# Performance work log

Hardware: AMD Instinct MI355X
Metric: run time of the kernel (lower is better)

## Reference

```python
import jax, jax.numpy as jnp
import numpy as np

B, T, D = 2, 2048, 1024
H, HS = 16, 64
EPS = 1e-5

def _ln(x, g, b):
    m = jnp.mean(x, axis=-1, keepdims=True)
    v = jnp.mean((x - m) ** 2, axis=-1, keepdims=True)
    return (x - m) * jax.lax.rsqrt(v + EPS) * g + b

def setup_inputs() -> dict:
    key = jax.random.key(0)
    ks = jax.random.split(key, 8)
    s_in = 1.0 / np.sqrt(D)
    s_ff = 1.0 / np.sqrt(4 * D)
    return {
        "embds": jax.random.normal(ks[0], (B, T, D), jnp.float32),
        "Wq": jax.random.normal(ks[1], (H, D, HS), jnp.float32) * s_in,
        "Wk": jax.random.normal(ks[2], (H, D, HS), jnp.float32) * s_in,
        "Wv": jax.random.normal(ks[3], (H, D, HS), jnp.float32) * s_in,
        "ln1_g": jnp.ones((D,), jnp.float32),
        "ln1_b": jnp.zeros((D,), jnp.float32),
        "ln2_g": jnp.ones((D,), jnp.float32),
        "ln2_b": jnp.zeros((D,), jnp.float32),
        "W1": jax.random.normal(ks[4], (D, 4 * D), jnp.float32) * s_in,
        "b1": jnp.zeros((4 * D,), jnp.float32),
        "W2": jax.random.normal(ks[5], (4 * D, D), jnp.float32) * s_ff,
        "b2": jnp.zeros((D,), jnp.float32),
    }

def reference(embds, Wq, Wk, Wv, ln1_g, ln1_b, ln2_g, ln2_b, W1, b1, W2, b2):
    _, t, d = embds.shape
    x = _ln(embds, ln1_g, ln1_b)
    q = jnp.einsum("btd,hde->bhte", x, Wq)
    k = jnp.einsum("btd,hde->bhte", x, Wk)
    v = jnp.einsum("btd,hde->bhte", x, Wv)
    # NOTE: repo scales by num_embds**-0.5 (C of input), not head_size**-0.5
    scores = jnp.einsum("bhte,bhse->bhts", q, k) * (d ** -0.5)
    causal = jnp.tril(jnp.ones((t, t), bool))
    scores = jnp.where(causal, scores, -jnp.inf)
    w = jax.nn.softmax(scores, axis=-1)
    o = jnp.einsum("bhts,bhse->bhte", w, v)  # [B,H,T,HS]
    attn = o.transpose(0, 2, 1, 3).reshape(embds.shape[0], t, -1)  # concat heads
    embds = embds + attn
    y = _ln(embds, ln2_g, ln2_b)
    ff = jax.nn.relu(y @ W1 + b1) @ W2 + b2
    return embds + ff
```

## Files before the change

### kernel.cpp

```cpp
#include <hip/hip_runtime.h>

using s16x8 = __attribute__((ext_vector_type(8))) short;
using f32x4 = __attribute__((ext_vector_type(4))) float;
typedef unsigned int   u32;
typedef unsigned short u16;

__device__ __forceinline__ u16 f2bf(float f) {
  u32 u = __float_as_uint(f);
  u += 0x7fffu + ((u >> 16) & 1u);
  return (u16)(u >> 16);
}
__device__ __forceinline__ float bf2f(u16 s) {
  return __uint_as_float(((u32)s) << 16);
}

typedef __attribute__((address_space(1))) const unsigned int g_u32;
typedef __attribute__((address_space(3))) unsigned int l_u32;
__device__ __forceinline__ void gload16(const void* g, void* l) {
  __builtin_amdgcn_global_load_lds((g_u32*)g, (l_u32*)l, 16, 0, 0);
}

#define WAITB(N) asm volatile("s_waitcnt vmcnt(" #N ")\ns_barrier" ::: "memory")
#define BAR()    asm volatile("s_barrier" ::: "memory")

__device__ __forceinline__ size_t kfrag_addr(int bh, int t, int e) {
  const int pair = (((t >> 4) & 3) << 1) + (e >> 5);
  const int slot = ((e >> 3) & 3) * 16 + (t & 15);
  return ((((size_t)bh * 32 + (t >> 6)) * 8 + pair) * 64 + slot) * 8 + (e & 7);
}
__device__ __forceinline__ size_t vfrag_addr(int bh, int t, int e) {
  const int pair = (((e >> 4) & 3) << 1) + ((t >> 5) & 1);
  const int slot = ((t >> 3) & 3) * 16 + (e & 15);
  return ((((size_t)bh * 32 + (t >> 6)) * 8 + pair) * 64 + slot) * 8 + (t & 7);
}

__global__ __launch_bounds__(256) void transpose_pack(
    const float* __restrict__ src, u16* __restrict__ dst, int R, int C)
{
  __shared__ u16 tile[64][66];
  const int tid = threadIdx.x;
  const int c0 = blockIdx.x * 64, r0 = blockIdx.y * 64;
  const size_t zoff = (size_t)blockIdx.z * R * C;
  src += zoff; dst += zoff;
  const int rr = tid >> 6, cc = tid & 63;
  #pragma unroll
  for (int i = 0; i < 16; ++i)
    tile[i * 4 + rr][cc] = f2bf(src[(size_t)(r0 + i * 4 + rr) * C + c0 + cc]);
  __syncthreads();
  #pragma unroll
  for (int i = 0; i < 16; ++i)
    dst[(size_t)(c0 + i * 4 + rr) * R + r0 + cc] = tile[cc][i * 4 + rr];
}

__global__ __launch_bounds__(256) void transpose_qkv(
    const float* __restrict__ Wq, const float* __restrict__ Wk,
    const float* __restrict__ Wv, u16* __restrict__ dst)
{
  __shared__ u16 tile[64][66];
  const int tid = threadIdx.x;
  const int sel = blockIdx.z >> 4, head = blockIdx.z & 15;
  const int r0 = blockIdx.y * 64;
  const float* src = ((sel == 0) ? Wq : (sel == 1) ? Wk : Wv) + (size_t)head * 65536;
  u16* d = dst + ((size_t)sel << 20) + (size_t)head * 65536;
  const int rr = tid >> 6, cc = tid & 63;
  #pragma unroll
  for (int i = 0; i < 16; ++i)
    tile[i * 4 + rr][cc] = f2bf(src[(size_t)(r0 + i * 4 + rr) * 64 + cc]);
  __syncthreads();
  #pragma unroll
  for (int i = 0; i < 16; ++i)
    d[(size_t)(i * 4 + rr) * 1024 + r0 + cc] = tile[cc][i * 4 + rr];
}

__global__ __launch_bounds__(256) void ln_kernel(
    const float* __restrict__ x, const float* __restrict__ g,
    const float* __restrict__ be, u16* __restrict__ out)
{
  const int row = blockIdx.x, tid = threadIdx.x;
  const int lane = tid & 63, wave = tid >> 6;
  const float4 v = ((const float4*)(x + (size_t)row * 1024))[tid];
  float s  = v.x + v.y + v.z + v.w;
  float sq = v.x * v.x + v.y * v.y + v.z * v.z + v.w * v.w;
  #pragma unroll
  for (int m = 1; m < 64; m <<= 1) { s += __shfl_xor(s, m); sq += __shfl_xor(sq, m); }
  __shared__ float rs[4], rq[4];
  if (lane == 0) { rs[wave] = s; rq[wave] = sq; }
  __syncthreads();
  s  = rs[0] + rs[1] + rs[2] + rs[3];
  sq = rq[0] + rq[1] + rq[2] + rq[3];
  const float mean = s * (1.0f / 1024.0f);
  const float var  = sq * (1.0f / 1024.0f) - mean * mean;
  const float rstd = rsqrtf(var + 1e-5f);
  const int c = tid * 4;
  const float4 gv = ((const float4*)g)[tid];
  const float4 bv = ((const float4*)be)[tid];
  ushort4 o;
  o.x = f2bf((v.x - mean) * rstd * gv.x + bv.x);
  o.y = f2bf((v.y - mean) * rstd * gv.y + bv.y);
  o.z = f2bf((v.z - mean) * rstd * gv.z + bv.z);
  o.w = f2bf((v.w - mean) * rstd * gv.w + bv.w);
  *(ushort4*)&out[(size_t)row * 1024 + c] = o;
}

#define MFMA_Q(MQ, NH)                                                        \
  do {                                                                        \
    __builtin_amdgcn_s_setprio(1);                                            \
    _Pragma("unroll") for (int m_ = 0; m_ < 4; ++m_)                          \
      _Pragma("unroll") for (int n_ = 0; n_ < 2; ++n_)                        \
        _Pragma("unroll") for (int ks_ = 0; ks_ < 2; ++ks_)                   \
          acc[MQ * 4 + m_][NH * 2 + n_] =                                     \
            __builtin_amdgcn_mfma_f32_16x16x32_bf16(                          \
              aF[m_][ks_], (NH ? b1F : b0F)[n_][ks_],                         \
              acc[MQ * 4 + m_][NH * 2 + n_], 0, 0, 0);                        \
    __builtin_amdgcn_s_setprio(0);                                            \
  } while (0)

template<int MODE>
__global__ __launch_bounds__(512, 2) void gemm256(
    const u16* __restrict__ A, int lda, const u16* __restrict__ BT, int ldb,
    int K, u16* __restrict__ o1, const float* __restrict__ bias,
    u16* __restrict__ pout)
{
  __shared__ alignas(16) u16 lds[2][2][256 * 64];
  const int tid = threadIdx.x, lane = tid & 63, w = tid >> 6;
  const int wm = w >> 2, wn = w & 3;
  const int fr = lane & 15, g = lane >> 4;
  const int gx = gridDim.x, nwg = gx * gridDim.y;
  int lid = blockIdx.y * gx + blockIdx.x;
  lid = (lid & 7) * (nwg >> 3) + (lid >> 3);
  const int col0 = (lid % gx) * 256, row0 = (lid / gx) * 256;
  const int koff = (MODE == 3) ? blockIdx.z * 1024 : 0;
  if constexpr (MODE == 3) pout += (size_t)blockIdx.z * (4096 * 1024);

  const int srow = w * 16 + (lane >> 3);
  const int scol8 = (lane & 7) ^ ((lane >> 3) & 7);
  const u16* Ab = A  + (size_t)(row0 + srow) * lda + koff + scol8 * 8;
  const u16* Bb = BT + (size_t)(col0 + srow) * ldb + koff + scol8 * 8;
  const int sdst = (w * 16) * 64 + lane * 8;

  const int x7 = fr & 7;
  const int rA = wm * 128 + fr;
  const int rB = wn * 64 + fr;

  f32x4 acc[8][4] = {};
  s16x8 aF[4][2], b0F[2][2], b1F[2][2];
  const int nkt = K >> 6;

  auto stA = [&](int buf, int half, int kt) {
    #pragma unroll
    for (int g2 = 0; g2 < 2; ++g2)
      gload16(Ab + (size_t)(half * 128 + g2 * 8) * lda + kt * 64,
              &lds[buf][0][(half * 128 + g2 * 8) * 64 + sdst]);
  };
  auto stB = [&](int buf, int half, int kt) {
    #pragma unroll
    for (int g2 = 0; g2 < 2; ++g2)
      gload16(Bb + (size_t)(half * 128 + g2 * 8) * ldb + kt * 64,
              &lds[buf][1][(half * 128 + g2 * 8) * 64 + sdst]);
  };
  auto rdA = [&](int buf, int mq) {
    #pragma unroll
    for (int m = 0; m < 4; ++m)
      #pragma unroll
      for (int ks = 0; ks < 2; ++ks)
        aF[m][ks] = *(const s16x8*)
          &lds[buf][0][(rA + mq * 64 + m * 16) * 64 + ((ks * 4 + g) ^ x7) * 8];
  };
  auto rdB0 = [&](int buf) {
    #pragma unroll
    for (int n = 0; n < 2; ++n)
      #pragma unroll
      for (int ks = 0; ks < 2; ++ks)
        b0F[n][ks] = *(const s16x8*)
          &lds[buf][1][(rB + n * 16) * 64 + ((ks * 4 + g) ^ x7) * 8];
  };
  auto rdB1 = [&](int buf) {
    #pragma unroll
    for (int n = 0; n < 2; ++n)
      #pragma unroll
      for (int ks = 0; ks < 2; ++ks)
        b1F[n][ks] = *(const s16x8*)
          &lds[buf][1][(rB + (n + 2) * 16) * 64 + ((ks * 4 + g) ^ x7) * 8];
  };

  stA(0, 0, 0); stA(0, 1, 0); stB(0, 0, 0); stB(0, 1, 0);
  stA(1, 0, 1); stA(1, 1, 1); stB(1, 0, 1); stB(1, 1, 1);
  WAITB(8);

  const int niter = nkt >> 1;
  for (int i = 0; i < niter; ++i) {
    #pragma unroll
    for (int half = 0; half < 2; ++half) {
      const int buf = half;
      const int skt = 2 * i + 2 + half;
      const bool st = (skt < nkt);
      rdA(buf, 0); rdB0(buf);
      BAR();
      MFMA_Q(0, 0);
      BAR();
      rdB1(buf);
      if (st) stB(buf, 0, skt);
      BAR();
      MFMA_Q(0, 1);
      BAR();
      rdA(buf, 1);
      if (st) stA(buf, 0, skt);
      BAR();
      MFMA_Q(1, 0);
      BAR();
      if (st) { stA(buf, 1, skt); stB(buf, 1, skt); }
      BAR();
      MFMA_Q(1, 1);
      WAITB(6);
    }
  }

  #pragma unroll
  for (int m8 = 0; m8 < 8; ++m8) {
    const int rbase = row0 + wm * 128 + m8 * 16 + g * 4;
    #pragma unroll
    for (int n4 = 0; n4 < 4; ++n4) {
      const int col = col0 + wn * 64 + n4 * 16 + fr;
      if constexpr (MODE == 1) {
        const float bb = bias[col];
        #pragma unroll
        for (int j = 0; j < 4; ++j)
          o1[(size_t)(rbase + j) * 4096 + col] =
            f2bf(fmaxf(acc[m8][n4][j] + bb, 0.0f));
      } else {
        #pragma unroll
        for (int j = 0; j < 4; ++j)
          pout[(size_t)(rbase + j) * 1024 + col] = f2bf(acc[m8][n4][j]);
      }
    }
  }
}

__global__ __launch_bounds__(256) void ff2_reduce(
    const u16* __restrict__ pbuf, const float* __restrict__ e2,
    const float* __restrict__ b2, float* __restrict__ out)
{
  const int i4 = blockIdx.x * 256 + threadIdx.x;
  const int row = i4 >> 8, c4 = i4 & 255;
  float4 a = ((const float4*)e2)[i4];
  const float4 bb = ((const float4*)b2)[c4];
  a.x += bb.x; a.y += bb.y; a.z += bb.z; a.w += bb.w;
  #pragma unroll
  for (int z = 0; z < 4; ++z) {
    const ushort4 p = *(const ushort4*)
      &pbuf[(size_t)z * (4096 * 1024) + (size_t)row * 1024 + c4 * 4];
    a.x += bf2f(p.x); a.y += bf2f(p.y); a.z += bf2f(p.z); a.w += bf2f(p.w);
  }
  ((float4*)out)[i4] = a;
}

template<int MODE, int MR>
__global__ __launch_bounds__(256) void gemm128(
    const u16* __restrict__ A, const u16* __restrict__ BT, int K,
    u16* __restrict__ o0q, u16* __restrict__ o0k, u16* __restrict__ o0v,
    u16* __restrict__ o1, const float* __restrict__ bias,
    float* __restrict__ o2, const float* __restrict__ resid)
{
  constexpr int BM = 64 * MR;
  __shared__ alignas(16) u16 As[3][BM * 32];
  __shared__ alignas(16) u16 Bs[3][128 * 32];
  const int tid = threadIdx.x, lane = tid & 63, wave = tid >> 6;
  const int wr = wave >> 1, wc = wave & 1;
  const int gx = gridDim.x;
  const int nwg = gx * gridDim.y;
  int lid = blockIdx.y * gx + blockIdx.x;
  lid = (lid & 7) * (nwg >> 3) + (lid >> 3);
  const int row0 = (lid / gx) * BM, col0 = (lid % gx) * 128;
  const int fr = lane & 15, g = lane >> 4;
  const int swz = (g ^ ((fr >> 1) & 3)) * 8;

  const int sr = wave * 16 + (lane >> 2);
  const int sc = ((lane & 3) ^ ((lane >> 3) & 3)) * 8;
  const u16* Ap0 = A  + (size_t)(row0 + sr) * K + sc;
  const u16* Ap1 = A  + (size_t)(row0 + 64 + sr) * K + sc;
  const u16* Bp0 = BT + (size_t)(col0 + sr) * K + sc;
  const u16* Bp1 = BT + (size_t)(col0 + 64 + sr) * K + sc;

  f32x4 acc[2 * MR][4] = {};

  auto stage = [&](int sel, int k0) {
    gload16(Ap0 + k0, &As[sel][wave * 512]);
    if constexpr (MR == 2) gload16(Ap1 + k0, &As[sel][(4 + wave) * 512]);
    gload16(Bp0 + k0, &Bs[sel][wave * 512]);
    gload16(Bp1 + k0, &Bs[sel][(4 + wave) * 512]);
  };
  auto compute = [&](int sel) {
    s16x8 af[2 * MR], bfr[4];
    #pragma unroll
    for (int m = 0; m < 2 * MR; ++m)
      af[m] = *(const s16x8*)&As[sel][(wr * (32 * MR) + m * 16 + fr) * 32 + swz];
    #pragma unroll
    for (int n = 0; n < 4; ++n)
      bfr[n] = *(const s16x8*)&Bs[sel][(wc * 64 + n * 16 + fr) * 32 + swz];
    #pragma unroll
    for (int m = 0; m < 2 * MR; ++m)
      #pragma unroll
      for (int n = 0; n < 4; ++n)
        acc[m][n] = __builtin_amdgcn_mfma_f32_16x16x32_bf16(af[m], bfr[n], acc[m][n], 0, 0, 0);
  };

  const int nsteps = K / 32;
  stage(0, 0);
  stage(1, 32);
  int cur = 0;
  for (int t = 0; t < nsteps - 1; ++t) {
    if constexpr (MR == 2) WAITB(4); else WAITB(3);
    const int nxt = (cur == 2) ? 0 : cur + 1;
    const int nn  = (nxt == 2) ? 0 : nxt + 1;
    if (t + 2 < nsteps) stage(nn, (t + 2) * 32);
    compute(cur);
    cur = nxt;
  }
  WAITB(0);
  compute(cur);

  const float QSCALE = 0.03125f * 1.4426950408889634f;
  #pragma unroll
  for (int m = 0; m < 2 * MR; ++m) {
    const int rbase = row0 + wr * (32 * MR) + m * 16 + g * 4;
    #pragma unroll
    for (int n = 0; n < 4; ++n) {
      const int col = col0 + wc * 64 + n * 16 + fr;
      if constexpr (MODE == 0) {
        const int ww = col >> 10, h = (col >> 6) & 15, e = col & 63;
        const int b = rbase >> 11, t0 = rbase & 2047;
        const int bh = b * 16 + h;
        if (ww == 0) {
          #pragma unroll
          for (int j = 0; j < 4; ++j)
            o0q[((size_t)bh * 2048 + (t0 + j)) * 64 + e] = f2bf(acc[m][n][j] * QSCALE);
        } else if (ww == 1) {
          #pragma unroll
          for (int j = 0; j < 4; ++j)
            o0k[kfrag_addr(bh, t0 + j, e)] = f2bf(acc[m][n][j]);
        } else {
          ushort4 pk;
          pk.x = f2bf(acc[m][n][0]); pk.y = f2bf(acc[m][n][1]);
          pk.z = f2bf(acc[m][n][2]); pk.w = f2bf(acc[m][n][3]);
          *(ushort4*)&o0v[vfrag_addr(bh, t0, e)] = pk;
        }
      } else if constexpr (MODE == 1) {
        const float bb = bias[col];
        #pragma unroll
        for (int j = 0; j < 4; ++j) {
          float v = fmaxf(acc[m][n][j] + bb, 0.0f);
          o1[(size_t)(rbase + j) * 4096 + col] = f2bf(v);
        }
      } else {
        const float bb = bias[col];
        #pragma unroll
        for (int j = 0; j < 4; ++j) {
          const size_t ix = (size_t)(rbase + j) * 1024 + col;
          o2[ix] = acc[m][n][j] + bb + resid[ix];
        }
      }
    }
  }
}

__global__ __launch_bounds__(256) void attn_mfma(
    const u16* __restrict__ q, const u16* __restrict__ kfragG,
    const u16* __restrict__ vfragG, const float* __restrict__ embds,
    float* __restrict__ e2)
{
  __shared__ alignas(16) u16 kbuf[3][4096];
  __shared__ alignas(16) u16 vbuf[3][4096];
  __shared__ alignas(16) u16 p_sm[4][16][72];
  const int tid = threadIdx.x, lane = tid & 63, wave = tid >> 6;
  const int bh = blockIdx.x & 31;
  const int qb = 31 - (blockIdx.x >> 5);
  const int q0 = qb * 64 + wave * 16;
  const int b = bh >> 4, h = bh & 15;
  const int fr = lane & 15, g = lane >> 4;

  const u16* qp = q + ((size_t)bh * 2048 + q0 + fr) * 64 + g * 8;
  const s16x8 qf0 = *(const s16x8*)(qp);
  const s16x8 qf1 = *(const s16x8*)(qp + 32);

  f32x4 o_acc[4] = {};
  float lacc[4] = {};

  const size_t fragbase = (size_t)bh * 131072;
  const int p0 = wave * 2, p1 = wave * 2 + 1;
  const int nch = qb + 1;

  auto stage_kv = [&](int sel, int c) {
    const size_t cb = fragbase + (size_t)c * 4096;
    gload16(kfragG + cb + p0 * 512 + lane * 8, &kbuf[sel][p0 * 512]);
    gload16(kfragG + cb + p1 * 512 + lane * 8, &kbuf[sel][p1 * 512]);
    gload16(vfragG + cb + p0 * 512 + lane * 8, &vbuf[sel][p0 * 512]);
    gload16(vfragG + cb + p1 * 512 + lane * 8, &vbuf[sel][p1 * 512]);
  };
  auto compute = [&](int sel, int s0) {
    f32x4 sacc[4] = {};
    #pragma unroll
    for (int n = 0; n < 4; ++n) {
      const s16x8 kf0 = *(const s16x8*)&kbuf[sel][(n * 2 + 0) * 512 + lane * 8];
      const s16x8 kf1 = *(const s16x8*)&kbuf[sel][(n * 2 + 1) * 512 + lane * 8];
      sacc[n] = __builtin_amdgcn_mfma_f32_16x16x32_bf16(qf0, kf0, sacc[n], 0, 0, 0);
      sacc[n] = __builtin_amdgcn_mfma_f32_16x16x32_bf16(qf1, kf1, sacc[n], 0, 0, 0);
    }
    if (s0 + 63 > q0) {
      #pragma unroll
      for (int n = 0; n < 4; ++n) {
        const int s = s0 + n * 16 + fr;
        #pragma unroll
        for (int j = 0; j < 4; ++j)
          if (s > q0 + g * 4 + j) sacc[n][j] = -1e30f;
      }
    }
    float p[4][4];
    #pragma unroll
    for (int n = 0; n < 4; ++n)
      #pragma unroll
      for (int j = 0; j < 4; ++j) {
        p[n][j] = __builtin_amdgcn_exp2f(sacc[n][j]);
        lacc[j] += p[n][j];
      }
    #pragma unroll
    for (int n = 0; n < 4; ++n)
      #pragma unroll
      for (int j = 0; j < 4; ++j)
        p_sm[wave][g * 4 + j][n * 16 + fr] = f2bf(p[n][j]);
    const s16x8 pf0 = *(const s16x8*)&p_sm[wave][fr][g * 8];
    const s16x8 pf1 = *(const s16x8*)&p_sm[wave][fr][32 + g * 8];
    #pragma unroll
    for (int n = 0; n < 4; ++n) {
      const s16x8 vf0 = *(const s16x8*)&vbuf[sel][(n * 2 + 0) * 512 + lane * 8];
      const s16x8 vf1 = *(const s16x8*)&vbuf[sel][(n * 2 + 1) * 512 + lane * 8];
      o_acc[n] = __builtin_amdgcn_mfma_f32_16x16x32_bf16(pf0, vf0, o_acc[n], 0, 0, 0);
      o_acc[n] = __builtin_amdgcn_mfma_f32_16x16x32_bf16(pf1, vf1, o_acc[n], 0, 0, 0);
    }
  };

  stage_kv(0, 0);
  if (nch > 1) stage_kv(1, 1);
  int cur = 0;
  for (int t = 0; t < nch - 1; ++t) {
    WAITB(4);
    const int nxt = (cur == 2) ? 0 : cur + 1;
    const int nn  = (nxt == 2) ? 0 : nxt + 1;
    if (t + 2 < nch) stage_kv(nn, t + 2);
    compute(cur, t * 64);
    cur = nxt;
  }
  WAITB(0);
  compute(cur, (nch - 1) * 64);

  #pragma unroll
  for (int j = 0; j < 4; ++j) {
    #pragma unroll
    for (int mm = 1; mm < 16; mm <<= 1) lacc[j] += __shfl_xor(lacc[j], mm);
  }
  #pragma unroll
  for (int n = 0; n < 4; ++n) {
    #pragma unroll
    for (int j = 0; j < 4; ++j) {
      const int t = q0 + g * 4 + j;
      const size_t oi = ((size_t)b * 2048 + t) * 1024 + (size_t)h * 64 + n * 16 + fr;
      e2[oi] = embds[oi] + o_acc[n][j] / lacc[j];
    }
  }
}

extern "C" void kernel_launch(void* const* d_in, const int* in_sizes, int n_in,
                              void* d_out, int out_size, void* d_ws, size_t ws_size,
                              hipStream_t stream) {
  const float* embds = (const float*)d_in[0];
  const float* Wq    = (const float*)d_in[1];
  const float* Wk    = (const float*)d_in[2];
  const float* Wv    = (const float*)d_in[3];
  const float* ln1g  = (const float*)d_in[4];
  const float* ln1b  = (const float*)d_in[5];
  const float* ln2g  = (const float*)d_in[6];
  const float* ln2b  = (const float*)d_in[7];
  const float* W1    = (const float*)d_in[8];
  const float* b1    = (const float*)d_in[9];
  const float* W2    = (const float*)d_in[10];
  const float* b2    = (const float*)d_in[11];
  float* out = (float*)d_out;

  char* ws = (char*)d_ws;
  u16*   xln   = (u16*)(ws);
  u16*   pbuf  = (u16*)(ws);
  u16*   wqkvT = (u16*)(ws + (8ull  << 20));
  u16*   qbuf  = (u16*)(ws + (14ull << 20));
  u16*   kfrag = (u16*)(ws + (22ull << 20));
  u16*   vfrag = (u16*)(ws + (30ull << 20));
  float* e2    = (float*)(ws + (38ull << 20));
  u16*   ybuf  = (u16*)(ws + (54ull << 20));
  u16*   w1T   = (u16*)(ws + (62ull << 20));
  u16*   w2T   = (u16*)(ws + (70ull << 20));
  u16*   hid   = (u16*)(ws + (78ull << 20));

  transpose_qkv<<<dim3(1, 16, 48), 256, 0, stream>>>(Wq, Wk, Wv, wqkvT);
  transpose_pack<<<dim3(64, 16, 1), 256, 0, stream>>>(W1, w1T, 1024, 4096);
  transpose_pack<<<dim3(16, 64, 1), 256, 0, stream>>>(W2, w2T, 4096, 1024);
  ln_kernel<<<4096, 256, 0, stream>>>(embds, ln1g, ln1b, xln);
  gemm128<0, 2><<<dim3(24, 32), 256, 0, stream>>>(xln, wqkvT, 1024,
      qbuf, kfrag, vfrag, nullptr, nullptr, nullptr, nullptr);
  attn_mfma<<<1024, 256, 0, stream>>>(qbuf, kfrag, vfrag, embds, e2);
  ln_kernel<<<4096, 256, 0, stream>>>(e2, ln2g, ln2b, ybuf);
  gemm256<1><<<dim3(16, 16), 512, 0, stream>>>(ybuf, 1024, w1T, 1024, 1024,
      hid, b1, nullptr);
  gemm256<3><<<dim3(4, 16, 4), 512, 0, stream>>>(hid, 4096, w2T, 4096, 1024,
      nullptr, nullptr, pbuf);
  ff2_reduce<<<4096, 256, 0, stream>>>(pbuf, e2, b2, out);
}
```

Measured before the change: 190.6 us.

## Route QKV projection through gemm256 and widen attention blocks to 128 queries

The QKV projection now runs through the larger 256x256 gemm256 kernel with a new MODE 0 epilogue that scatters Q, K and V into their attention layouts, and the old gemm128 kernel is removed. The attention kernel now uses 512-thread blocks covering 128 query rows, so each staged K/V chunk is shared by 8 waves instead of 4. K/V buffering drops from triple to double, with a full wait at each step. The aim is more reuse of operands and fewer blocks, at the cost of a shallower prefetch pipeline in attention and a coarser grid (192 blocks) for the QKV GEMM.

```diff
diff --git a/kernel.cpp b/kernel.cpp
--- a/kernel.cpp
+++ b/kernel.cpp
@@ -119,7 +119,8 @@
 __global__ __launch_bounds__(512, 2) void gemm256(
     const u16* __restrict__ A, int lda, const u16* __restrict__ BT, int ldb,
     int K, u16* __restrict__ o1, const float* __restrict__ bias,
-    u16* __restrict__ pout)
+    u16* __restrict__ pout, u16* __restrict__ o0q, u16* __restrict__ o0k,
+    u16* __restrict__ o0v)
 {
   __shared__ alignas(16) u16 lds[2][2][256 * 64];
   const int tid = threadIdx.x, lane = tid & 63, w = tid >> 6;
@@ -215,13 +216,33 @@
     }
   }
 
+  const float QSCALE = 0.03125f * 1.4426950408889634f;
   #pragma unroll
   for (int m8 = 0; m8 < 8; ++m8) {
     const int rbase = row0 + wm * 128 + m8 * 16 + g * 4;
     #pragma unroll
     for (int n4 = 0; n4 < 4; ++n4) {
       const int col = col0 + wn * 64 + n4 * 16 + fr;
-      if constexpr (MODE == 1) {
+      if constexpr (MODE == 0) {
+        const int ww = col >> 10, h = (col >> 6) & 15, e = col & 63;
+        const int b = rbase >> 11, t0 = rbase & 2047;
+        const int bh = b * 16 + h;
+        if (ww == 0) {
+          #pragma unroll
+          for (int j = 0; j < 4; ++j)
+            o0q[((size_t)bh * 2048 + (t0 + j)) * 64 + e] =
+              f2bf(acc[m8][n4][j] * QSCALE);
+        } else if (ww == 1) {
+          #pragma unroll
+          for (int j = 0; j < 4; ++j)
+            o0k[kfrag_addr(bh, t0 + j, e)] = f2bf(acc[m8][n4][j]);
+        } else {
+          ushort4 pk;
+          pk.x = f2bf(acc[m8][n4][0]); pk.y = f2bf(acc[m8][n4][1]);
+          pk.z = f2bf(acc[m8][n4][2]); pk.w = f2bf(acc[m8][n4][3]);
+          *(ushort4*)&o0v[vfrag_addr(bh, t0, e)] = pk;
+        }
+      } else if constexpr (MODE == 1) {
         const float bb = bias[col];
         #pragma unroll
         for (int j = 0; j < 4; ++j)
@@ -254,127 +275,18 @@
   ((float4*)out)[i4] = a;
 }
 
-template<int MODE, int MR>
-__global__ __launch_bounds__(256) void gemm128(
-    const u16* __restrict__ A, const u16* __restrict__ BT, int K,
-    u16* __restrict__ o0q, u16* __restrict__ o0k, u16* __restrict__ o0v,
-    u16* __restrict__ o1, const float* __restrict__ bias,
-    float* __restrict__ o2, const float* __restrict__ resid)
-{
-  constexpr int BM = 64 * MR;
-  __shared__ alignas(16) u16 As[3][BM * 32];
-  __shared__ alignas(16) u16 Bs[3][128 * 32];
-  const int tid = threadIdx.x, lane = tid & 63, wave = tid >> 6;
-  const int wr = wave >> 1, wc = wave & 1;
-  const int gx = gridDim.x;
-  const int nwg = gx * gridDim.y;
-  int lid = blockIdx.y * gx + blockIdx.x;
-  lid = (lid & 7) * (nwg >> 3) + (lid >> 3);
-  const int row0 = (lid / gx) * BM, col0 = (lid % gx) * 128;
-  const int fr = lane & 15, g = lane >> 4;
-  const int swz = (g ^ ((fr >> 1) & 3)) * 8;
-
-  const int sr = wave * 16 + (lane >> 2);
-  const int sc = ((lane & 3) ^ ((lane >> 3) & 3)) * 8;
-  const u16* Ap0 = A  + (size_t)(row0 + sr) * K + sc;
-  const u16* Ap1 = A  + (size_t)(row0 + 64 + sr) * K + sc;
-  const u16* Bp0 = BT + (size_t)(col0 + sr) * K + sc;
-  const u16* Bp1 = BT + (size_t)(col0 + 64 + sr) * K + sc;
-
-  f32x4 acc[2 * MR][4] = {};
-
-  auto stage = [&](int sel, int k0) {
-    gload16(Ap0 + k0, &As[sel][wave * 512]);
-    if constexpr (MR == 2) gload16(Ap1 + k0, &As[sel][(4 + wave) * 512]);
-    gload16(Bp0 + k0, &Bs[sel][wave * 512]);
-    gload16(Bp1 + k0, &Bs[sel][(4 + wave) * 512]);
-  };
-  auto compute = [&](int sel) {
-    s16x8 af[2 * MR], bfr[4];
-    #pragma unroll
-    for (int m = 0; m < 2 * MR; ++m)
-      af[m] = *(const s16x8*)&As[sel][(wr * (32 * MR) + m * 16 + fr) * 32 + swz];
-    #pragma unroll
-    for (int n = 0; n < 4; ++n)
-      bfr[n] = *(const s16x8*)&Bs[sel][(wc * 64 + n * 16 + fr) * 32 + swz];
-    #pragma unroll
-    for (int m = 0; m < 2 * MR; ++m)
-      #pragma unroll
-      for (int n = 0; n < 4; ++n)
-        acc[m][n] = __builtin_amdgcn_mfma_f32_16x16x32_bf16(af[m], bfr[n], acc[m][n], 0, 0, 0);
-  };
-
-  const int nsteps = K / 32;
-  stage(0, 0);
-  stage(1, 32);
-  int cur = 0;
-  for (int t = 0; t < nsteps - 1; ++t) {
-    if constexpr (MR == 2) WAITB(4); else WAITB(3);
-    const int nxt = (cur == 2) ? 0 : cur + 1;
-    const int nn  = (nxt == 2) ? 0 : nxt + 1;
-    if (t + 2 < nsteps) stage(nn, (t + 2) * 32);
-    compute(cur);
-    cur = nxt;
-  }
-  WAITB(0);
-  compute(cur);
-
-  const float QSCALE = 0.03125f * 1.4426950408889634f;
-  #pragma unroll
-  for (int m = 0; m < 2 * MR; ++m) {
-    const int rbase = row0 + wr * (32 * MR) + m * 16 + g * 4;
-    #pragma unroll
-    for (int n = 0; n < 4; ++n) {
-      const int col = col0 + wc * 64 + n * 16 + fr;
-      if constexpr (MODE == 0) {
-        const int ww = col >> 10, h = (col >> 6) & 15, e = col & 63;
-        const int b = rbase >> 11, t0 = rbase & 2047;
-        const int bh = b * 16 + h;
-        if (ww == 0) {
-          #pragma unroll
-          for (int j = 0; j < 4; ++j)
-            o0q[((size_t)bh * 2048 + (t0 + j)) * 64 + e] = f2bf(acc[m][n][j] * QSCALE);
-        } else if (ww == 1) {
-          #pragma unroll
-          for (int j = 0; j < 4; ++j)
-            o0k[kfrag_addr(bh, t0 + j, e)] = f2bf(acc[m][n][j]);
-        } else {
-          ushort4 pk;
-          pk.x = f2bf(acc[m][n][0]); pk.y = f2bf(acc[m][n][1]);
-          pk.z = f2bf(acc[m][n][2]); pk.w = f2bf(acc[m][n][3]);
-          *(ushort4*)&o0v[vfrag_addr(bh, t0, e)] = pk;
-        }
-      } else if constexpr (MODE == 1) {
-        const float bb = bias[col];
-        #pragma unroll
-        for (int j = 0; j < 4; ++j) {
-          float v = fmaxf(acc[m][n][j] + bb, 0.0f);
-          o1[(size_t)(rbase + j) * 4096 + col] = f2bf(v);
-        }
-      } else {
-        const float bb = bias[col];
-        #pragma unroll
-        for (int j = 0; j < 4; ++j) {
-          const size_t ix = (size_t)(rbase + j) * 1024 + col;
-          o2[ix] = acc[m][n][j] + bb + resid[ix];
-        }
-      }
-    }
-  }
-}
-
-__global__ __launch_bounds__(256) void attn_mfma(
+__global__ __launch_bounds__(512, 6) void attn_mfma(
     const u16* __restrict__ q, const u16* __restrict__ kfragG,
     const u16* __restrict__ vfragG, const float* __restrict__ embds,
     float* __restrict__ e2)
 {
-  __shared__ alignas(16) u16 kbuf[3][4096];
-  __shared__ alignas(16) u16 vbuf[3][4096];
-  __shared__ alignas(16) u16 p_sm[4][16][72];
+  __shared__ alignas(16) u16 kbuf[2][4096];
+  __shared__ alignas(16) u16 vbuf[2][4096];
+  __shared__ alignas(16) u16 p_sm[8][16][72];
   const int tid = threadIdx.x, lane = tid & 63, wave = tid >> 6;
   const int bh = blockIdx.x & 31;
-  const int qb = 31 - (blockIdx.x >> 5);
-  const int q0 = qb * 64 + wave * 16;
+  const int qb = 15 - (blockIdx.x >> 5);
+  const int q0 = qb * 128 + wave * 16;
   const int b = bh >> 4, h = bh & 15;
   const int fr = lane & 15, g = lane >> 4;
 
@@ -386,15 +298,12 @@
   float lacc[4] = {};
 
   const size_t fragbase = (size_t)bh * 131072;
-  const int p0 = wave * 2, p1 = wave * 2 + 1;
-  const int nch = qb + 1;
+  const int nch = qb * 2 + 2;
 
   auto stage_kv = [&](int sel, int c) {
     const size_t cb = fragbase + (size_t)c * 4096;
-    gload16(kfragG + cb + p0 * 512 + lane * 8, &kbuf[sel][p0 * 512]);
-    gload16(kfragG + cb + p1 * 512 + lane * 8, &kbuf[sel][p1 * 512]);
-    gload16(vfragG + cb + p0 * 512 + lane * 8, &vbuf[sel][p0 * 512]);
-    gload16(vfragG + cb + p1 * 512 + lane * 8, &vbuf[sel][p1 * 512]);
+    gload16(kfragG + cb + wave * 512 + lane * 8, &kbuf[sel][wave * 512]);
+    gload16(vfragG + cb + wave * 512 + lane * 8, &vbuf[sel][wave * 512]);
   };
   auto compute = [&](int sel, int s0) {
     f32x4 sacc[4] = {};
@@ -414,19 +323,14 @@
           if (s > q0 + g * 4 + j) sacc[n][j] = -1e30f;
       }
     }
-    float p[4][4];
     #pragma unroll
     for (int n = 0; n < 4; ++n)
       #pragma unroll
       for (int j = 0; j < 4; ++j) {
-        p[n][j] = __builtin_amdgcn_exp2f(sacc[n][j]);
-        lacc[j] += p[n][j];
+        const float pe = __builtin_amdgcn_exp2f(sacc[n][j]);
+        lacc[j] += pe;
+        p_sm[wave][g * 4 + j][n * 16 + fr] = f2bf(pe);
       }
-    #pragma unroll
-    for (int n = 0; n < 4; ++n)
-      #pragma unroll
-      for (int j = 0; j < 4; ++j)
-        p_sm[wave][g * 4 + j][n * 16 + fr] = f2bf(p[n][j]);
     const s16x8 pf0 = *(const s16x8*)&p_sm[wave][fr][g * 8];
     const s16x8 pf1 = *(const s16x8*)&p_sm[wave][fr][32 + g * 8];
     #pragma unroll
@@ -439,18 +343,11 @@
   };
 
   stage_kv(0, 0);
-  if (nch > 1) stage_kv(1, 1);
-  int cur = 0;
-  for (int t = 0; t < nch - 1; ++t) {
-    WAITB(4);
-    const int nxt = (cur == 2) ? 0 : cur + 1;
-    const int nn  = (nxt == 2) ? 0 : nxt + 1;
-    if (t + 2 < nch) stage_kv(nn, t + 2);
-    compute(cur, t * 64);
-    cur = nxt;
-  }
-  WAITB(0);
-  compute(cur, (nch - 1) * 64);
+  for (int t = 0; t < nch; ++t) {
+    WAITB(0);
+    if (t + 1 < nch) stage_kv((t + 1) & 1, t + 1);
+    compute(t & 1, t * 64);
+  }
 
   #pragma unroll
   for (int j = 0; j < 4; ++j) {
@@ -502,13 +399,13 @@
   transpose_pack<<<dim3(64, 16, 1), 256, 0, stream>>>(W1, w1T, 1024, 4096);
   transpose_pack<<<dim3(16, 64, 1), 256, 0, stream>>>(W2, w2T, 4096, 1024);
   ln_kernel<<<4096, 256, 0, stream>>>(embds, ln1g, ln1b, xln);
-  gemm128<0, 2><<<dim3(24, 32), 256, 0, stream>>>(xln, wqkvT, 1024,
-      qbuf, kfrag, vfrag, nullptr, nullptr, nullptr, nullptr);
-  attn_mfma<<<1024, 256, 0, stream>>>(qbuf, kfrag, vfrag, embds, e2);
+  gemm256<0><<<dim3(12, 16), 512, 0, stream>>>(xln, 1024, wqkvT, 1024, 1024,
+      nullptr, nullptr, nullptr, qbuf, kfrag, vfrag);
+  attn_mfma<<<512, 512, 0, stream>>>(qbuf, kfrag, vfrag, embds, e2);
   ln_kernel<<<4096, 256, 0, stream>>>(e2, ln2g, ln2b, ybuf);
   gemm256<1><<<dim3(16, 16), 512, 0, stream>>>(ybuf, 1024, w1T, 1024, 1024,
-      hid, b1, nullptr);
+      hid, b1, nullptr, nullptr, nullptr, nullptr);
   gemm256<3><<<dim3(4, 16, 4), 512, 0, stream>>>(hid, 4096, w2T, 4096, 1024,
-      nullptr, nullptr, pbuf);
+      nullptr, nullptr, pbuf, nullptr, nullptr, nullptr);
   ff2_reduce<<<4096, 256, 0, stream>>>(pbuf, e2, b2, out);
 }
```

Measured after the change: 191.5 us. No clear change (+0.4%).

## Double attention query tile to 128 rows with 8 waves and double-buffered KV

Applied to the files above, without the earlier changes.

The attention kernel now runs 512 threads (8 waves) per block, covering 128 query rows instead of 64, so each staged K/V chunk is shared by twice as many waves. The KV pipeline drops from triple to double buffering with a full wait each iteration, and each wave issues one load per K and V chunk. The exp/store loop is fused so probabilities go straight to LDS. This halves global K/V traffic per query but weakens prefetch depth, and for the diagonal block the extra chunk is computed fully masked for half the waves. The gemm256 and reduce kernels were only moved in the file.

```diff
diff --git a/kernel.cpp b/kernel.cpp
--- a/kernel.cpp
+++ b/kernel.cpp
@@ -100,158 +100,6 @@
   o.z = f2bf((v.z - mean) * rstd * gv.z + bv.z);
   o.w = f2bf((v.w - mean) * rstd * gv.w + bv.w);
   *(ushort4*)&out[(size_t)row * 1024 + c] = o;
-}
-
-#define MFMA_Q(MQ, NH)                                                        \
-  do {                                                                        \
-    __builtin_amdgcn_s_setprio(1);                                            \
-    _Pragma("unroll") for (int m_ = 0; m_ < 4; ++m_)                          \
-      _Pragma("unroll") for (int n_ = 0; n_ < 2; ++n_)                        \
-        _Pragma("unroll") for (int ks_ = 0; ks_ < 2; ++ks_)                   \
-          acc[MQ * 4 + m_][NH * 2 + n_] =                                     \
-            __builtin_amdgcn_mfma_f32_16x16x32_bf16(                          \
-              aF[m_][ks_], (NH ? b1F : b0F)[n_][ks_],                         \
-              acc[MQ * 4 + m_][NH * 2 + n_], 0, 0, 0);                        \
-    __builtin_amdgcn_s_setprio(0);                                            \
-  } while (0)
-
-template<int MODE>
-__global__ __launch_bounds__(512, 2) void gemm256(
-    const u16* __restrict__ A, int lda, const u16* __restrict__ BT, int ldb,
-    int K, u16* __restrict__ o1, const float* __restrict__ bias,
-    u16* __restrict__ pout)
-{
-  __shared__ alignas(16) u16 lds[2][2][256 * 64];
-  const int tid = threadIdx.x, lane = tid & 63, w = tid >> 6;
-  const int wm = w >> 2, wn = w & 3;
-  const int fr = lane & 15, g = lane >> 4;
-  const int gx = gridDim.x, nwg = gx * gridDim.y;
-  int lid = blockIdx.y * gx + blockIdx.x;
-  lid = (lid & 7) * (nwg >> 3) + (lid >> 3);
-  const int col0 = (lid % gx) * 256, row0 = (lid / gx) * 256;
-  const int koff = (MODE == 3) ? blockIdx.z * 1024 : 0;
-  if constexpr (MODE == 3) pout += (size_t)blockIdx.z * (4096 * 1024);
-
-  const int srow = w * 16 + (lane >> 3);
-  const int scol8 = (lane & 7) ^ ((lane >> 3) & 7);
-  const u16* Ab = A  + (size_t)(row0 + srow) * lda + koff + scol8 * 8;
-  const u16* Bb = BT + (size_t)(col0 + srow) * ldb + koff + scol8 * 8;
-  const int sdst = (w * 16) * 64 + lane * 8;
-
-  const int x7 = fr & 7;
-  const int rA = wm * 128 + fr;
-  const int rB = wn * 64 + fr;
-
-  f32x4 acc[8][4] = {};
-  s16x8 aF[4][2], b0F[2][2], b1F[2][2];
-  const int nkt = K >> 6;
-
-  auto stA = [&](int buf, int half, int kt) {
-    #pragma unroll
-    for (int g2 = 0; g2 < 2; ++g2)
-      gload16(Ab + (size_t)(half * 128 + g2 * 8) * lda + kt * 64,
-              &lds[buf][0][(half * 128 + g2 * 8) * 64 + sdst]);
-  };
-  auto stB = [&](int buf, int half, int kt) {
-    #pragma unroll
-    for (int g2 = 0; g2 < 2; ++g2)
-      gload16(Bb + (size_t)(half * 128 + g2 * 8) * ldb + kt * 64,
-              &lds[buf][1][(half * 128 + g2 * 8) * 64 + sdst]);
-  };
-  auto rdA = [&](int buf, int mq) {
-    #pragma unroll
-    for (int m = 0; m < 4; ++m)
-      #pragma unroll
-      for (int ks = 0; ks < 2; ++ks)
-        aF[m][ks] = *(const s16x8*)
-          &lds[buf][0][(rA + mq * 64 + m * 16) * 64 + ((ks * 4 + g) ^ x7) * 8];
-  };
-  auto rdB0 = [&](int buf) {
-    #pragma unroll
-    for (int n = 0; n < 2; ++n)
-      #pragma unroll
-      for (int ks = 0; ks < 2; ++ks)
-        b0F[n][ks] = *(const s16x8*)
-          &lds[buf][1][(rB + n * 16) * 64 + ((ks * 4 + g) ^ x7) * 8];
-  };
-  auto rdB1 = [&](int buf) {
-    #pragma unroll
-    for (int n = 0; n < 2; ++n)
-      #pragma unroll
-      for (int ks = 0; ks < 2; ++ks)
-        b1F[n][ks] = *(const s16x8*)
-          &lds[buf][1][(rB + (n + 2) * 16) * 64 + ((ks * 4 + g) ^ x7) * 8];
-  };
-
-  stA(0, 0, 0); stA(0, 1, 0); stB(0, 0, 0); stB(0, 1, 0);
-  stA(1, 0, 1); stA(1, 1, 1); stB(1, 0, 1); stB(1, 1, 1);
-  WAITB(8);
-
-  const int niter = nkt >> 1;
-  for (int i = 0; i < niter; ++i) {
-    #pragma unroll
-    for (int half = 0; half < 2; ++half) {
-      const int buf = half;
-      const int skt = 2 * i + 2 + half;
-      const bool st = (skt < nkt);
-      rdA(buf, 0); rdB0(buf);
-      BAR();
-      MFMA_Q(0, 0);
-      BAR();
-      rdB1(buf);
-      if (st) stB(buf, 0, skt);
-      BAR();
-      MFMA_Q(0, 1);
-      BAR();
-      rdA(buf, 1);
-      if (st) stA(buf, 0, skt);
-      BAR();
-      MFMA_Q(1, 0);
-      BAR();
-      if (st) { stA(buf, 1, skt); stB(buf, 1, skt); }
-      BAR();
-      MFMA_Q(1, 1);
-      WAITB(6);
-    }
-  }
-
-  #pragma unroll
-  for (int m8 = 0; m8 < 8; ++m8) {
-    const int rbase = row0 + wm * 128 + m8 * 16 + g * 4;
-    #pragma unroll
-    for (int n4 = 0; n4 < 4; ++n4) {
-      const int col = col0 + wn * 64 + n4 * 16 + fr;
-      if constexpr (MODE == 1) {
-        const float bb = bias[col];
-        #pragma unroll
-        for (int j = 0; j < 4; ++j)
-          o1[(size_t)(rbase + j) * 4096 + col] =
-            f2bf(fmaxf(acc[m8][n4][j] + bb, 0.0f));
-      } else {
-        #pragma unroll
-        for (int j = 0; j < 4; ++j)
-          pout[(size_t)(rbase + j) * 1024 + col] = f2bf(acc[m8][n4][j]);
-      }
-    }
-  }
-}
-
-__global__ __launch_bounds__(256) void ff2_reduce(
-    const u16* __restrict__ pbuf, const float* __restrict__ e2,
-    const float* __restrict__ b2, float* __restrict__ out)
-{
-  const int i4 = blockIdx.x * 256 + threadIdx.x;
-  const int row = i4 >> 8, c4 = i4 & 255;
-  float4 a = ((const float4*)e2)[i4];
-  const float4 bb = ((const float4*)b2)[c4];
-  a.x += bb.x; a.y += bb.y; a.z += bb.z; a.w += bb.w;
-  #pragma unroll
-  for (int z = 0; z < 4; ++z) {
-    const ushort4 p = *(const ushort4*)
-      &pbuf[(size_t)z * (4096 * 1024) + (size_t)row * 1024 + c4 * 4];
-    a.x += bf2f(p.x); a.y += bf2f(p.y); a.z += bf2f(p.z); a.w += bf2f(p.w);
-  }
-  ((float4*)out)[i4] = a;
 }
 
 template<int MODE, int MR>
@@ -363,18 +211,170 @@
   }
 }
 
-__global__ __launch_bounds__(256) void attn_mfma(
+#define MFMA_Q(MQ, NH)                                                        \
+  do {                                                                        \
+    __builtin_amdgcn_s_setprio(1);                                            \
+    _Pragma("unroll") for (int m_ = 0; m_ < 4; ++m_)                          \
+      _Pragma("unroll") for (int n_ = 0; n_ < 2; ++n_)                        \
+        _Pragma("unroll") for (int ks_ = 0; ks_ < 2; ++ks_)                   \
+          acc[MQ * 4 + m_][NH * 2 + n_] =                                     \
+            __builtin_amdgcn_mfma_f32_16x16x32_bf16(                          \
+              aF[m_][ks_], (NH ? b1F : b0F)[n_][ks_],                         \
+              acc[MQ * 4 + m_][NH * 2 + n_], 0, 0, 0);                        \
+    __builtin_amdgcn_s_setprio(0);                                            \
+  } while (0)
+
+template<int MODE>
+__global__ __launch_bounds__(512, 2) void gemm256(
+    const u16* __restrict__ A, int lda, const u16* __restrict__ BT, int ldb,
+    int K, u16* __restrict__ o1, const float* __restrict__ bias,
+    u16* __restrict__ pout)
+{
+  __shared__ alignas(16) u16 lds[2][2][256 * 64];
+  const int tid = threadIdx.x, lane = tid & 63, w = tid >> 6;
+  const int wm = w >> 2, wn = w & 3;
+  const int fr = lane & 15, g = lane >> 4;
+  const int gx = gridDim.x, nwg = gx * gridDim.y;
+  int lid = blockIdx.y * gx + blockIdx.x;
+  lid = (lid & 7) * (nwg >> 3) + (lid >> 3);
+  const int col0 = (lid % gx) * 256, row0 = (lid / gx) * 256;
+  const int koff = (MODE == 3) ? blockIdx.z * 1024 : 0;
+  if constexpr (MODE == 3) pout += (size_t)blockIdx.z * (4096 * 1024);
+
+  const int srow = w * 16 + (lane >> 3);
+  const int scol8 = (lane & 7) ^ ((lane >> 3) & 7);
+  const u16* Ab = A  + (size_t)(row0 + srow) * lda + koff + scol8 * 8;
+  const u16* Bb = BT + (size_t)(col0 + srow) * ldb + koff + scol8 * 8;
+  const int sdst = (w * 16) * 64 + lane * 8;
+
+  const int x7 = fr & 7;
+  const int rA = wm * 128 + fr;
+  const int rB = wn * 64 + fr;
+
+  f32x4 acc[8][4] = {};
+  s16x8 aF[4][2], b0F[2][2], b1F[2][2];
+  const int nkt = K >> 6;
+
+  auto stA = [&](int buf, int half, int kt) {
+    #pragma unroll
+    for (int g2 = 0; g2 < 2; ++g2)
+      gload16(Ab + (size_t)(half * 128 + g2 * 8) * lda + kt * 64,
+              &lds[buf][0][(half * 128 + g2 * 8) * 64 + sdst]);
+  };
+  auto stB = [&](int buf, int half, int kt) {
+    #pragma unroll
+    for (int g2 = 0; g2 < 2; ++g2)
+      gload16(Bb + (size_t)(half * 128 + g2 * 8) * ldb + kt * 64,
+              &lds[buf][1][(half * 128 + g2 * 8) * 64 + sdst]);
+  };
+  auto rdA = [&](int buf, int mq) {
+    #pragma unroll
+    for (int m = 0; m < 4; ++m)
+      #pragma unroll
+      for (int ks = 0; ks < 2; ++ks)
+        aF[m][ks] = *(const s16x8*)
+          &lds[buf][0][(rA + mq * 64 + m * 16) * 64 + ((ks * 4 + g) ^ x7) * 8];
+  };
+  auto rdB0 = [&](int buf) {
+    #pragma unroll
+    for (int n = 0; n < 2; ++n)
+      #pragma unroll
+      for (int ks = 0; ks < 2; ++ks)
+        b0F[n][ks] = *(const s16x8*)
+          &lds[buf][1][(rB + n * 16) * 64 + ((ks * 4 + g) ^ x7) * 8];
+  };
+  auto rdB1 = [&](int buf) {
+    #pragma unroll
+    for (int n = 0; n < 2; ++n)
+      #pragma unroll
+      for (int ks = 0; ks < 2; ++ks)
+        b1F[n][ks] = *(const s16x8*)
+          &lds[buf][1][(rB + (n + 2) * 16) * 64 + ((ks * 4 + g) ^ x7) * 8];
+  };
+
+  stA(0, 0, 0); stA(0, 1, 0); stB(0, 0, 0); stB(0, 1, 0);
+  stA(1, 0, 1); stA(1, 1, 1); stB(1, 0, 1); stB(1, 1, 1);
+  WAITB(8);
+
+  const int niter = nkt >> 1;
+  for (int i = 0; i < niter; ++i) {
+    #pragma unroll
+    for (int half = 0; half < 2; ++half) {
+      const int buf = half;
+      const int skt = 2 * i + 2 + half;
+      const bool st = (skt < nkt);
+      rdA(buf, 0); rdB0(buf);
+      BAR();
+      MFMA_Q(0, 0);
+      BAR();
+      rdB1(buf);
+      if (st) stB(buf, 0, skt);
+      BAR();
+      MFMA_Q(0, 1);
+      BAR();
+      rdA(buf, 1);
+      if (st) stA(buf, 0, skt);
+      BAR();
+      MFMA_Q(1, 0);
+      BAR();
+      if (st) { stA(buf, 1, skt); stB(buf, 1, skt); }
+      BAR();
+      MFMA_Q(1, 1);
+      WAITB(6);
+    }
+  }
+
+  #pragma unroll
+  for (int m8 = 0; m8 < 8; ++m8) {
+    const int rbase = row0 + wm * 128 + m8 * 16 + g * 4;
+    #pragma unroll
+    for (int n4 = 0; n4 < 4; ++n4) {
+      const int col = col0 + wn * 64 + n4 * 16 + fr;
+      if constexpr (MODE == 1) {
+        const float bb = bias[col];
+        #pragma unroll
+        for (int j = 0; j < 4; ++j)
+          o1[(size_t)(rbase + j) * 4096 + col] =
+            f2bf(fmaxf(acc[m8][n4][j] + bb, 0.0f));
+      } else {
+        #pragma unroll
+        for (int j = 0; j < 4; ++j)
+          pout[(size_t)(rbase + j) * 1024 + col] = f2bf(acc[m8][n4][j]);
+      }
+    }
+  }
+}
+
+__global__ __launch_bounds__(256) void ff2_reduce(
+    const u16* __restrict__ pbuf, const float* __restrict__ e2,
+    const float* __restrict__ b2, float* __restrict__ out)
+{
+  const int i4 = blockIdx.x * 256 + threadIdx.x;
+  const int row = i4 >> 8, c4 = i4 & 255;
+  float4 a = ((const float4*)e2)[i4];
+  const float4 bb = ((const float4*)b2)[c4];
+  a.x += bb.x; a.y += bb.y; a.z += bb.z; a.w += bb.w;
+  #pragma unroll
+  for (int z = 0; z < 4; ++z) {
+    const ushort4 p = *(const ushort4*)
+      &pbuf[(size_t)z * (4096 * 1024) + (size_t)row * 1024 + c4 * 4];
+    a.x += bf2f(p.x); a.y += bf2f(p.y); a.z += bf2f(p.z); a.w += bf2f(p.w);
+  }
+  ((float4*)out)[i4] = a;
+}
+
+__global__ __launch_bounds__(512, 6) void attn_mfma(
     const u16* __restrict__ q, const u16* __restrict__ kfragG,
     const u16* __restrict__ vfragG, const float* __restrict__ embds,
     float* __restrict__ e2)
 {
-  __shared__ alignas(16) u16 kbuf[3][4096];
-  __shared__ alignas(16) u16 vbuf[3][4096];
-  __shared__ alignas(16) u16 p_sm[4][16][72];
+  __shared__ alignas(16) u16 kbuf[2][4096];
+  __shared__ alignas(16) u16 vbuf[2][4096];
+  __shared__ alignas(16) u16 p_sm[8][16][72];
   const int tid = threadIdx.x, lane = tid & 63, wave = tid >> 6;
   const int bh = blockIdx.x & 31;
-  const int qb = 31 - (blockIdx.x >> 5);
-  const int q0 = qb * 64 + wave * 16;
+  const int qb = 15 - (blockIdx.x >> 5);
+  const int q0 = qb * 128 + wave * 16;
   const int b = bh >> 4, h = bh & 15;
   const int fr = lane & 15, g = lane >> 4;
 
@@ -386,15 +386,12 @@
   float lacc[4] = {};
 
   const size_t fragbase = (size_t)bh * 131072;
-  const int p0 = wave * 2, p1 = wave * 2 + 1;
-  const int nch = qb + 1;
+  const int nch = qb * 2 + 2;
 
   auto stage_kv = [&](int sel, int c) {
     const size_t cb = fragbase + (size_t)c * 4096;
-    gload16(kfragG + cb + p0 * 512 + lane * 8, &kbuf[sel][p0 * 512]);
-    gload16(kfragG + cb + p1 * 512 + lane * 8, &kbuf[sel][p1 * 512]);
-    gload16(vfragG + cb + p0 * 512 + lane * 8, &vbuf[sel][p0 * 512]);
-    gload16(vfragG + cb + p1 * 512 + lane * 8, &vbuf[sel][p1 * 512]);
+    gload16(kfragG + cb + wave * 512 + lane * 8, &kbuf[sel][wave * 512]);
+    gload16(vfragG + cb + wave * 512 + lane * 8, &vbuf[sel][wave * 512]);
   };
   auto compute = [&](int sel, int s0) {
     f32x4 sacc[4] = {};
@@ -414,19 +411,14 @@
           if (s > q0 + g * 4 + j) sacc[n][j] = -1e30f;
       }
     }
-    float p[4][4];
     #pragma unroll
     for (int n = 0; n < 4; ++n)
       #pragma unroll
       for (int j = 0; j < 4; ++j) {
-        p[n][j] = __builtin_amdgcn_exp2f(sacc[n][j]);
-        lacc[j] += p[n][j];
+        const float pe = __builtin_amdgcn_exp2f(sacc[n][j]);
+        lacc[j] += pe;
+        p_sm[wave][g * 4 + j][n * 16 + fr] = f2bf(pe);
       }
-    #pragma unroll
-    for (int n = 0; n < 4; ++n)
-      #pragma unroll
-      for (int j = 0; j < 4; ++j)
-        p_sm[wave][g * 4 + j][n * 16 + fr] = f2bf(p[n][j]);
     const s16x8 pf0 = *(const s16x8*)&p_sm[wave][fr][g * 8];
     const s16x8 pf1 = *(const s16x8*)&p_sm[wave][fr][32 + g * 8];
     #pragma unroll
@@ -439,18 +431,11 @@
   };
 
   stage_kv(0, 0);
-  if (nch > 1) stage_kv(1, 1);
-  int cur = 0;
-  for (int t = 0; t < nch - 1; ++t) {
-    WAITB(4);
-    const int nxt = (cur == 2) ? 0 : cur + 1;
-    const int nn  = (nxt == 2) ? 0 : nxt + 1;
-    if (t + 2 < nch) stage_kv(nn, t + 2);
-    compute(cur, t * 64);
-    cur = nxt;
-  }
-  WAITB(0);
-  compute(cur, (nch - 1) * 64);
+  for (int t = 0; t < nch; ++t) {
+    WAITB(0);
+    if (t + 1 < nch) stage_kv((t + 1) & 1, t + 1);
+    compute(t & 1, t * 64);
+  }
 
   #pragma unroll
   for (int j = 0; j < 4; ++j) {
@@ -504,7 +489,7 @@
   ln_kernel<<<4096, 256, 0, stream>>>(embds, ln1g, ln1b, xln);
   gemm128<0, 2><<<dim3(24, 32), 256, 0, stream>>>(xln, wqkvT, 1024,
       qbuf, kfrag, vfrag, nullptr, nullptr, nullptr, nullptr);
-  attn_mfma<<<1024, 256, 0, stream>>>(qbuf, kfrag, vfrag, embds, e2);
+  attn_mfma<<<512, 512, 0, stream>>>(qbuf, kfrag, vfrag, embds, e2);
   ln_kernel<<<4096, 256, 0, stream>>>(e2, ln2g, ln2b, ybuf);
   gemm256<1><<<dim3(16, 16), 512, 0, stream>>>(ybuf, 1024, w1T, 1024, 1024,
       hid, b1, nullptr);
```

New measurement: 189.4 us. About the same (-0.6%).
